# Performance work log

Measured on AMD Instinct MI355X. Metric: run time of the kernel, lower is better.

The kernel has to match this reference:

```python
import jax, jax.numpy as jnp
import numpy as np

MEAN = 0.1307
SIGMA = 0.3081
BINARY_ITER = 10
SIG_SCALE = 5.0


def spu(x):
    # SPU(x) = x^2 - 0.5 for x >= 0, sigmoid(-x) - 1 for x < 0 (continuous at 0)
    return jnp.where(x >= 0, x * x - 0.5, jax.nn.sigmoid(-x) - 1.0)


def joining_line(x1, y1, x2, y2):
    slope = (y2 - y1) / (x2 - x1)
    return slope, y2 - slope * x2


def parabola_tangent(x):
    return 2.0 * x, -x * x - 0.5


def parabola_tangent_through(x1, y1):
    D = 4.0 * x1 * x1 - 4.0 * y1 - 2.0
    x2 = (2.0 * x1 + jnp.sqrt(jnp.clip(D, 0.0))) / 2.0
    return parabola_tangent(x2)


def sigmoid_tangent(x):
    s = jax.nn.sigmoid(x)
    slope = -s * (1.0 - s)
    return slope, -s - slope * x


def binary_search_point(lx, ux, uy):
    L = lx
    R = jnp.zeros_like(lx)
    for _ in range(BINARY_ITER):  # fixed 10-iteration search, unrolled
        m = 0.5 * (L + R)
        sm, im = sigmoid_tangent(m)
        mask = sm * ux + im - uy > 0
        L = jnp.where(mask, m, L)
        R = jnp.where(mask, R, m)
    return L


def line_to_constraint(slope, intercept):
    # [n, n+1]: diagonal slope matrix with intercept as last column (matches torch diagflat/cat)
    return jnp.concatenate([jnp.diagflat(slope), intercept[:, None]], axis=1)


def analyze_affine(W, b, ub, lb):
    constr = jnp.concatenate([W, b[:, None]], axis=1)
    bu = jnp.where(W > 0, ub[None, :], lb[None, :])
    bl = jnp.where(W > 0, lb[None, :], ub[None, :])
    return constr, jnp.einsum('ij,ij->i', bu, W) + b, jnp.einsum('ij,ij->i', bl, W) + b


def analyze_spu(ux, lx):
    uy = spu(ux)
    ly = spu(lx)
    new_ub = jnp.maximum(uy, ly)
    sj, ij = joining_line(lx, ly, ux, uy)
    right = lx > 0
    left = ux <= 0
    crossing = (~left) & (~right)
    # learned positions at their (fresh) init: sigmoid(0) -> midpoint
    mid = 0.5 * (ux + lx)
    sp, ip = parabola_tangent(mid)
    ssm, ism = sigmoid_tangent(mid)
    new_lb = jnp.where(crossing, jnp.full_like(uy, -0.5), jnp.minimum(uy, ly))
    # crossing-case lower constraint
    spu_, ipu = parabola_tangent(ux)
    limit = spu_ * lx + ipu
    clm = (jnp.abs(lx) > ux).astype(lx.dtype)
    clp = jax.nn.sigmoid((clm - 0.5) * 2.0 * SIG_SCALE) * (ly - limit) + limit
    ptm = clp < -0.5
    spt, ipt = parabola_tangent_through(lx, clp)
    sjn, ijn = joining_line(lx, clp, jnp.zeros_like(lx), jnp.full_like(lx, -0.5))
    s_cl = jnp.where(ptm, spt, sjn)
    i_cl = jnp.where(ptm, ipt, ijn)
    # crossing-case upper constraint
    ssl, isl = sigmoid_tangent(lx)
    stv = ssl * ux + isl - uy
    L = binary_search_point(lx, ux, uy)
    scp = jax.nn.sigmoid(-SIG_SCALE) * (L - lx) + lx
    ssc, isc = sigmoid_tangent(scp)
    up_mask = stv > 0
    s_cu = jnp.where(up_mask, ssc, sj)
    i_cu = jnp.where(up_mask, isc, ij)
    rf = right.astype(lx.dtype)
    lf = left.astype(lx.dtype)
    cf = crossing.astype(lx.dtype)
    us = rf * sj + lf * ssm + cf * s_cu
    ui = rf * ij + lf * ism + cf * i_cu
    ls = rf * sp + lf * sj + cf * s_cl
    li = rf * ip + lf * ij + cf * i_cl
    return line_to_constraint(us, ui), line_to_constraint(ls, li), new_ub, new_lb


def back_substitute(uc, lc, ub, lb):
    cu, cl = uc[-1], lc[-1]
    for pu, pl in zip(uc[-2::-1], lc[-2::-1]):
        # where(curr>0, prev_upper, prev_lower) contracted with curr == split pos/neg matmuls
        Wu, bu = cu[:, :-1], cu[:, -1]
        cu = jnp.maximum(Wu, 0.0) @ pu + jnp.minimum(Wu, 0.0) @ pl
        cu = cu.at[:, -1].add(bu)
        Wl, bl = cl[:, :-1], cl[:, -1]
        cl = jnp.maximum(Wl, 0.0) @ pl + jnp.minimum(Wl, 0.0) @ pu
        cl = cl.at[:, -1].add(bl)
    return jnp.minimum(ub, cu[:, 0]), jnp.maximum(lb, cl[:, 0])


def setup_inputs() -> dict:
    key = jax.random.key(0)
    ks = jax.random.split(key, 9)
    d_in, h, d_out = 784, 2048, 10
    inputs = jax.random.uniform(ks[0], (d_in,), dtype=jnp.float32)
    eps = jnp.float32(0.05)
    w1 = jax.random.normal(ks[1], (h, d_in), dtype=jnp.float32) / np.sqrt(d_in).astype(np.float32)
    b1 = jax.random.normal(ks[2], (h,), dtype=jnp.float32) * 0.1
    w2 = jax.random.normal(ks[3], (h, h), dtype=jnp.float32) / np.sqrt(h).astype(np.float32)
    b2 = jax.random.normal(ks[4], (h,), dtype=jnp.float32) * 0.1
    w3 = jax.random.normal(ks[5], (h, h), dtype=jnp.float32) / np.sqrt(h).astype(np.float32)
    b3 = jax.random.normal(ks[6], (h,), dtype=jnp.float32) * 0.1
    w4 = jax.random.normal(ks[7], (d_out, h), dtype=jnp.float32) / np.sqrt(h).astype(np.float32)
    b4 = jax.random.normal(ks[8], (d_out,), dtype=jnp.float32) * 0.1
    return {"inputs": inputs, "eps": eps, "w1": w1, "b1": b1, "w2": w2, "b2": b2,
            "w3": w3, "b3": b3, "w4": w4, "b4": b4}


def reference(inputs, eps, w1, b1, w2, b2, w3, b3, w4, b4):
    ub = [jnp.clip(inputs + eps, None, 1.0)]
    lb = [jnp.clip(inputs - eps, 0.0)]
    # normalization layer: applied in place to bounds and input constraint ([784,1])
    uc = [((ub[0] - MEAN) / SIGMA)[:, None]]
    lc = [((lb[0] - MEAN) / SIGMA)[:, None]]
    ub[0] = (ub[0] - MEAN) / SIGMA
    lb[0] = (lb[0] - MEAN) / SIGMA
    weights = [(w1, b1), (w2, b2), (w3, b3), (w4, b4)]
    for i, (W, b) in enumerate(weights):
        c, u, l = analyze_affine(W, b, ub[-1], lb[-1])
        uc.append(c)
        lc.append(c)
        ub.append(u)
        lb.append(l)
        u, l = back_substitute(uc, lc, ub[-1], lb[-1])
        ub[-1], lb[-1] = u, l
        if i < len(weights) - 1:
            cu_, cl_, u, l = analyze_spu(ub[-1], lb[-1])
            uc.append(cu_)
            lc.append(cl_)
            ub.append(u)
            lb.append(l)
            u, l = back_substitute(uc, lc, ub[-1], lb[-1])
            ub[-1], lb[-1] = u, l
    return lb[-1].min()
```

## Files before the change

kernel.cpp:

```cpp
#include <hip/hip_runtime.h>
#include <cstdint>
#include <cstddef>

#define MEAN_C 0.1307f
#define SIGMA_C 0.3081f
#define SIG_SCALE_C 5.0f

typedef __bf16 bf16_t;
typedef __bf16 bf16x8 __attribute__((ext_vector_type(8)));
typedef __bf16 bf16x4 __attribute__((ext_vector_type(4)));
typedef float f32x4 __attribute__((ext_vector_type(4)));

__device__ __forceinline__ f32x4 mfma16(bf16x8 a, bf16x8 b, f32x4 c) {
    return __builtin_amdgcn_mfma_f32_16x16x32_bf16(a, b, c, 0, 0, 0);
}

typedef const __attribute__((address_space(1))) void* gvp;
typedef __attribute__((address_space(3))) void* lvp;
__device__ __forceinline__ void g2l16(const void* g, void* l) {
    __builtin_amdgcn_global_load_lds((gvp)g, (lvp)l, 16, 0, 0);
}

__device__ __forceinline__ size_t swz(int r, int k, int ktiles) {
    return (((size_t)(r >> 4) * ktiles + (k >> 5)) << 9)
         + (((k >> 3) & 3) << 7) + ((r & 15) << 3) + (k & 7);
}

#define KTILES 64


__device__ __forceinline__ float sigmoidf_(float x) {
    if (x >= 0.f) { float e = __expf(-x); return 1.f / (1.f + e); }
    float e = __expf(x); return e / (1.f + e);
}

__device__ __forceinline__ float spu_f(float x) {
    return (x >= 0.f) ? (x * x - 0.5f) : (sigmoidf_(-x) - 1.f);
}

__device__ __forceinline__ float wave_sum(float a) {
    #pragma unroll
    for (int o = 32; o > 0; o >>= 1) a += __shfl_xor(a, o, 64);
    return a;
}


__global__ __launch_bounds__(256) void k_interval_affine(
        const float* __restrict__ W, const float* __restrict__ b,
        const float* __restrict__ U, const float* __restrict__ L,
        int m, int nrows, float* __restrict__ uo, float* __restrict__ lo) {
    int r = (blockIdx.x << 2) + (threadIdx.x >> 6);
    if (r >= nrows) return;
    int lane = threadIdx.x & 63;
    const f32x4* Wr = (const f32x4*)(W + (size_t)r * m);
    const f32x4* U4 = (const f32x4*)U;
    const f32x4* L4 = (const f32x4*)L;
    int nf4 = m >> 2;
    float au = 0.f, al = 0.f;
    for (int j = lane; j < nf4; j += 64) {
        f32x4 wv = Wr[j], uu = U4[j], ll = L4[j];
        #pragma unroll
        for (int u = 0; u < 4; ++u) {
            float w = wv[u];
            float hi = (w > 0.f) ? uu[u] : ll[u];
            float lo2 = (w > 0.f) ? ll[u] : uu[u];
            au = fmaf(w, hi, au);
            al = fmaf(w, lo2, al);
        }
    }
    au = wave_sum(au); al = wave_sum(al);
    if (lane == 0) { uo[r] = au + b[r]; lo[r] = al + b[r]; }
}

__global__ void k_spu2(const float* __restrict__ iU, const float* __restrict__ iL,
                       const float* __restrict__ vraw, int n,
                       float* __restrict__ us, float* __restrict__ ui,
                       float* __restrict__ ls, float* __restrict__ li,
                       float* __restrict__ pU, float* __restrict__ pL) {
    int i = blockIdx.x * blockDim.x + threadIdx.x;
    if (i >= n) return;
    float ux = fminf(iU[i], vraw[i]);
    float lx = fmaxf(iL[i], vraw[n + i]);
    float uy = spu_f(ux), ly = spu_f(lx);
    float new_ub = fmaxf(uy, ly);
    float sj = (uy - ly) / (ux - lx);
    float ij = uy - sj * ux;
    bool right = lx > 0.f;
    bool left = ux <= 0.f;
    bool crossing = (!left) && (!right);
    float mid = 0.5f * (ux + lx);
    float sp = 2.f * mid, ip = -mid * mid - 0.5f;
    float sm = sigmoidf_(mid);
    float ssm = -sm * (1.f - sm);
    float ism = -sm - ssm * mid;
    float new_lb = crossing ? -0.5f : fminf(uy, ly);
    float spu_s = 2.f * ux, ipu = -ux * ux - 0.5f;
    float limit = spu_s * lx + ipu;
    float clm = (fabsf(lx) > ux) ? 1.f : 0.f;
    float clp = sigmoidf_((clm - 0.5f) * 2.f * SIG_SCALE_C) * (ly - limit) + limit;
    bool ptm = clp < -0.5f;
    float D = 4.f * lx * lx - 4.f * clp - 2.f;
    float x2 = (2.f * lx + sqrtf(fmaxf(D, 0.f))) * 0.5f;
    float spt = 2.f * x2, ipt = -x2 * x2 - 0.5f;
    float sjn = (clp + 0.5f) / lx;
    float ijn = -0.5f;
    float s_cl = ptm ? spt : sjn;
    float i_cl = ptm ? ipt : ijn;
    float sl = sigmoidf_(lx);
    float ssl = -sl * (1.f - sl);
    float isl = -sl - ssl * lx;
    float stv = ssl * ux + isl - uy;
    float Lb = lx, Rb = 0.f;
    #pragma unroll
    for (int t = 0; t < 10; ++t) {
        float mm = 0.5f * (Lb + Rb);
        float smm = sigmoidf_(mm);
        float sms = -smm * (1.f - smm);
        float smi = -smm - sms * mm;
        bool mask = (sms * ux + smi - uy) > 0.f;
        Lb = mask ? mm : Lb;
        Rb = mask ? Rb : mm;
    }
    float scp = sigmoidf_(-SIG_SCALE_C) * (Lb - lx) + lx;
    float sc = sigmoidf_(scp);
    float ssc = -sc * (1.f - sc);
    float isc = -sc - ssc * scp;
    bool up = stv > 0.f;
    float s_cu = up ? ssc : sj;
    float i_cu = up ? isc : ij;
    float usv, uiv, lsv, liv;
    if (right)      { usv = sj;   uiv = ij;   lsv = sp;   liv = ip;   }
    else if (left)  { usv = ssm;  uiv = ism;  lsv = sj;   liv = ij;   }
    else            { usv = s_cu; uiv = i_cu; lsv = s_cl; liv = i_cl; }
    us[i] = usv; ui[i] = uiv; ls[i] = lsv; li[i] = liv;
    float vu = vraw[(usv >= 0.f) ? i : n + i];
    float vl = vraw[(lsv >= 0.f) ? n + i : i];
    pU[i] = fminf(new_ub, usv * vu + uiv);
    pL[i] = fmaxf(new_lb, lsv * vl + liv);
}


__global__ __launch_bounds__(256) void k_wT3(
        const float* __restrict__ W1, const float* __restrict__ W2,
        const float* __restrict__ W3,
        bf16_t* __restrict__ W1t, bf16_t* __restrict__ W2t, bf16_t* __restrict__ W3t,
        const float* __restrict__ x, const float* __restrict__ eps,
        float* __restrict__ ubn, float* __restrict__ lbn) {
    __shared__ bf16_t t[64][72];
    int z = blockIdx.z;
    const float* W; int N, ldw; bf16_t* Wt;
    if (z == 0)      { W = W2; N = 2048; ldw = 2048; Wt = W2t; }
    else if (z == 1) { W = W3; N = 2048; ldw = 2048; Wt = W3t; }
    else {
        W = W1; N = 784; ldw = 784; Wt = W1t;
        if (blockIdx.y >= 14) {
            if (blockIdx.y == 14 && blockIdx.x == 0) {
                for (int i = threadIdx.x; i < 896; i += 256) {
                    if (i >= 784) { ubn[i] = 0.f; lbn[i] = 0.f; }
                    else {
                        float e = eps[0];
                        float ub = fminf(x[i] + e, 1.f);
                        float lb = fmaxf(x[i] - e, 0.f);
                        ubn[i] = (ub - MEAN_C) / SIGMA_C;
                        lbn[i] = (lb - MEAN_C) / SIGMA_C;
                    }
                }
            }
            return;
        }
    }
    int k0 = blockIdx.x * 64, n0 = blockIdx.y * 64;
    int tid = threadIdx.x;
    int r = tid >> 2;
    int c0 = (tid & 3) * 16;
    const float* Wr = W + (size_t)(k0 + r) * ldw;
    #pragma unroll
    for (int c = 0; c < 16; ++c) {
        int gn = n0 + c0 + c;
        float vv = (gn < N) ? Wr[gn] : 0.f;
        t[c0 + c][r] = (bf16_t)vv;
    }
    __syncthreads();
    #pragma unroll
    for (int p = 0; p < 2; ++p) {
        int c = tid + p * 256;
        int lr = c & 63, lq = c >> 6;
        bf16x8 v;
        #pragma unroll
        for (int u = 0; u < 8; ++u) v[u] = t[lr][lq * 8 + u];
        *(bf16x8*)(Wt + swz(n0 + lr, k0 + lq * 8, KTILES)) = v;
    }
}

__global__ __launch_bounds__(256) void k_prep16(
        const float* __restrict__ W, const float* __restrict__ b, int n,
        const float* __restrict__ cus, const float* __restrict__ cui,
        const float* __restrict__ cls, const float* __restrict__ cli,
        const float* __restrict__ bvec,
        const float* __restrict__ U, const float* __restrict__ L,
        bf16_t* __restrict__ Ab, float* __restrict__ av,
        float* __restrict__ iU, float* __restrict__ iL) {
    int rt = blockIdx.x;
    int tid = threadIdx.x, lane = tid & 63, wid = tid >> 6;
    int mrow = lane & 15, q = lane >> 4;
    int r = rt * 16 + mrow;
    bool act = r < 2 * n;
    bool isU = r < n;
    int i = act ? (isU ? r : r - n) : 0;
    float gate = act ? 1.f : 0.f;
    const float* Wr = W + (size_t)i * 2048;
    const float* ps = isU ? cus : cls;
    const float* ns = isU ? cls : cus;
    const float* yi = isU ? cui : cli;
    const float* zi = isU ? cli : cui;
    const float* hi = isU ? U : L;
    const float* lo = isU ? L : U;
    float a = 0.f, a2 = 0.f;
    bf16_t* Abase = Ab + ((size_t)rt * KTILES) * 512 + lane * 8;
    for (int kt = wid; kt < KTILES; kt += 4) {
        int k0 = kt * 32 + q * 8;
        bf16x8 ov;
        #pragma unroll
        for (int h = 0; h < 2; ++h) {
            int kb = k0 + 4 * h;
            f32x4 wv = *(const f32x4*)(Wr + kb);
            f32x4 p0 = *(const f32x4*)(ps + kb);
            f32x4 q0 = *(const f32x4*)(ns + kb);
            f32x4 y0 = *(const f32x4*)(yi + kb);
            f32x4 z0 = *(const f32x4*)(zi + kb);
            f32x4 c0 = *(const f32x4*)(bvec + kb);
            f32x4 h0 = *(const f32x4*)(hi + kb);
            f32x4 l0 = *(const f32x4*)(lo + kb);
            #pragma unroll
            for (int u = 0; u < 4; ++u) {
                float w = gate * wv[u];
                float pos = fmaxf(w, 0.f), neg = fminf(w, 0.f);
                float mx = pos * p0[u] + neg * q0[u];
                ov[4 * h + u] = (bf16_t)mx;
                a += pos * y0[u] + neg * z0[u] + mx * c0[u];
                a2 += pos * h0[u] + neg * l0[u];
            }
        }
        *(bf16x8*)(Abase + (size_t)kt * 512) = ov;
    }
    a += __shfl_xor(a, 16, 64);  a += __shfl_xor(a, 32, 64);
    a2 += __shfl_xor(a2, 16, 64); a2 += __shfl_xor(a2, 32, 64);
    __shared__ float sh[2][4][16];
    if (lane < 16) { sh[0][wid][lane] = a; sh[1][wid][lane] = a2; }
    __syncthreads();
    if (tid < 16) {
        int r2 = rt * 16 + tid;
        float ta = sh[0][0][tid] + sh[0][1][tid] + sh[0][2][tid] + sh[0][3][tid];
        float tb = sh[1][0][tid] + sh[1][1][tid] + sh[1][2][tid] + sh[1][3][tid];
        if (r2 < 2 * n) {
            bool isU2 = r2 < n;
            int i2 = isU2 ? r2 : r2 - n;
            av[r2] = ta + b[i2];
            if (isU2) iU[i2] = tb + b[i2];
            else      iL[i2] = tb + b[i2];
        } else {
            av[r2] = 0.f;
        }
    }
}

__global__ __launch_bounds__(256) void k_colmix16(
        const bf16_t* __restrict__ Cb, int ldc, int splits, size_t sstride, int n,
        int tpb,
        const float* __restrict__ cus, const float* __restrict__ cui,
        const float* __restrict__ cls, const float* __restrict__ cli,
        const float* __restrict__ bvec,
        bf16_t* __restrict__ Ab, float* __restrict__ av) {
    int rt = blockIdx.x;
    int kt0 = blockIdx.y * tpb;
    int tid = threadIdx.x, lane = tid & 63, wid = tid >> 6;
    int mrow = lane & 15, q = lane >> 4;
    int r = rt * 16 + mrow;
    bool isU = r < n;
    const bf16_t* Cr = Cb + (size_t)r * ldc;
    const float* ps = isU ? cus : cls;
    const float* ns = isU ? cls : cus;
    const float* yi = isU ? cui : cli;
    const float* zi = isU ? cli : cui;
    float a = 0.f;
    bf16_t* Abase = Ab + ((size_t)rt * KTILES) * 512 + lane * 8;
    for (int kt = kt0 + wid; kt < kt0 + tpb; kt += 4) {
        int k0 = kt * 32 + q * 8;
        float wsum[8] = {0.f, 0.f, 0.f, 0.f, 0.f, 0.f, 0.f, 0.f};
        for (int s = 0; s < splits; ++s) {
            bf16x8 v = *(const bf16x8*)(Cr + s * sstride + k0);
            #pragma unroll
            for (int u = 0; u < 8; ++u) wsum[u] += (float)v[u];
        }
        f32x4 p0 = *(const f32x4*)(ps + k0), p1 = *(const f32x4*)(ps + k0 + 4);
        f32x4 q0 = *(const f32x4*)(ns + k0), q1 = *(const f32x4*)(ns + k0 + 4);
        f32x4 y0 = *(const f32x4*)(yi + k0), y1 = *(const f32x4*)(yi + k0 + 4);
        f32x4 z0 = *(const f32x4*)(zi + k0), z1 = *(const f32x4*)(zi + k0 + 4);
        f32x4 c0 = *(const f32x4*)(bvec + k0), c1 = *(const f32x4*)(bvec + k0 + 4);
        bf16x8 ov;
        #pragma unroll
        for (int u = 0; u < 4; ++u) {
            float w = wsum[u];
            float pos = fmaxf(w, 0.f), neg = fminf(w, 0.f);
            float mx = pos * p0[u] + neg * q0[u];
            ov[u] = (bf16_t)mx;
            a += pos * y0[u] + neg * z0[u] + mx * c0[u];
        }
        #pragma unroll
        for (int u = 0; u < 4; ++u) {
            float w = wsum[4 + u];
            float pos = fmaxf(w, 0.f), neg = fminf(w, 0.f);
            float mx = pos * p1[u] + neg * q1[u];
            ov[4 + u] = (bf16_t)mx;
            a += pos * y1[u] + neg * z1[u] + mx * c1[u];
        }
        *(bf16x8*)(Abase + (size_t)kt * 512) = ov;
    }
    a += __shfl_xor(a, 16, 64);
    a += __shfl_xor(a, 32, 64);
    __shared__ float sh[4][16];
    if (lane < 16) sh[wid][lane] = a;
    __syncthreads();
    if (tid < 16) {
        float tot = sh[0][tid] + sh[1][tid] + sh[2][tid] + sh[3][tid];
        atomicAdd(&av[rt * 16 + tid], tot);
    }
}

__global__ __launch_bounds__(640) void k_reduce16f(
        const bf16_t* __restrict__ Cb, int ldc, int m, int n,
        int splits, size_t sstride,
        const float* __restrict__ av,
        const float* __restrict__ ubn, const float* __restrict__ lbn,
        const float* __restrict__ iL,
        float* __restrict__ out) {
    __shared__ float sbl[16];
    int tid = threadIdx.x, lane = tid & 63, wv = tid >> 6;
    int nch = m >> 3;
    int i = wv;
    int r = n + i;
    const bf16_t* Cr = Cb + (size_t)r * ldc;
    const float* p = lbn;
    const float* q = ubn;
    float a = 0.f;
    for (int c = lane; c < nch; c += 64) {
        float wsum[8] = {0.f, 0.f, 0.f, 0.f, 0.f, 0.f, 0.f, 0.f};
        for (int s = 0; s < splits; ++s) {
            bf16x8 v = *(const bf16x8*)(Cr + s * sstride + c * 8);
            #pragma unroll
            for (int u = 0; u < 8; ++u) wsum[u] += (float)v[u];
        }
        f32x4 p0 = *(const f32x4*)(p + c * 8), p1 = *(const f32x4*)(p + c * 8 + 4);
        f32x4 q0 = *(const f32x4*)(q + c * 8), q1 = *(const f32x4*)(q + c * 8 + 4);
        #pragma unroll
        for (int u = 0; u < 4; ++u) {
            a += fmaxf(wsum[u], 0.f) * p0[u] + fminf(wsum[u], 0.f) * q0[u];
            a += fmaxf(wsum[4 + u], 0.f) * p1[u] + fminf(wsum[4 + u], 0.f) * q1[u];
        }
    }
    a = wave_sum(a);
    if (lane == 0) sbl[i] = fmaxf(iL[i], a + av[r]);
    __syncthreads();
    if (tid < 64) {
        float v = 3.4e38f;
        for (int j = lane; j < n; j += 64) v = fminf(v, sbl[j]);
        #pragma unroll
        for (int o = 32; o > 0; o >>= 1) v = fminf(v, __shfl_down(v, o, 64));
        if (lane == 0) out[0] = v;
    }
}


#define GEMM_PIPE()                                                            \
    int tid = threadIdx.x, lane = tid & 63, w = tid >> 6;                      \
    int wm = w & 1, wn = w >> 1;                                               \
    const int nsteps = nk * 2;                                                 \
    f32x4 acc[4][4];                                                           \
    _Pragma("unroll")                                                          \
    for (int i = 0; i < 4; ++i)                                                \
        _Pragma("unroll")                                                      \
        for (int j = 0; j < 4; ++j) acc[i][j] = (f32x4){0.f, 0.f, 0.f, 0.f};   \
    auto stage = [&](int js) {                                                 \
        int b = js & 3;                                                        \
        size_t go = (size_t)js * 512;                                          \
        bf16_t* la = &As4[b * 4096 + w * 512];                                 \
        bf16_t* lb = &Bs4[b * 4096 + w * 512];                                 \
        g2l16(a0 + go, la);   g2l16(a1 + go, la + 2048);                       \
        g2l16(b0 + go, lb);   g2l16(b1 + go, lb + 2048);                       \
    };                                                                         \
    stage(0); stage(1); stage(2);                                              \
    asm volatile("s_waitcnt vmcnt(8)" ::: "memory");                           \
    __builtin_amdgcn_s_barrier();                                              \
    for (int j = 0; j < nsteps; ++j) {                                         \
        int b = j & 3;                                                         \
        const bf16_t* cA = &As4[b * 4096];                                     \
        const bf16_t* cB = &Bs4[b * 4096];                                     \
        bf16x8 af[4], bq[4];                                                   \
        _Pragma("unroll")                                                      \
        for (int i = 0; i < 4; ++i) {                                          \
            af[i] = *(const bf16x8*)(cA + (wm * 4 + i) * 512 + lane * 8);      \
            bq[i] = *(const bf16x8*)(cB + (wn * 4 + i) * 512 + lane * 8);      \
        }                                                                      \
        if (j + 3 < nsteps) stage(j + 3);                                      \
        _Pragma("unroll")                                                      \
        for (int i = 0; i < 4; ++i)                                            \
            _Pragma("unroll")                                                  \
            for (int jj = 0; jj < 4; ++jj)                                     \
                acc[i][jj] = mfma16(bq[jj], af[i], acc[i][jj]);                \
        int rem = nsteps - 2 - j;                                              \
        if (rem >= 2)      asm volatile("s_waitcnt vmcnt(8)" ::: "memory");    \
        else if (rem == 1) asm volatile("s_waitcnt vmcnt(4)" ::: "memory");    \
        else               asm volatile("s_waitcnt vmcnt(0)" ::: "memory");    \
        __builtin_amdgcn_s_barrier();                                          \
    }

__global__ __launch_bounds__(256) void k_gemm16(
        const bf16_t* __restrict__ A, const bf16_t* __restrict__ Bt,
        bf16_t* __restrict__ C, int ldc, size_t sstride, int nk) {
    __shared__ __align__(16) bf16_t As4[16384];
    __shared__ __align__(16) bf16_t Bs4[16384];
    int tr0 = blockIdx.y * 8, tc0 = blockIdx.x * 8;
    int kt0 = blockIdx.z * nk * 2;
    int wtmp = threadIdx.x >> 6, ltmp = threadIdx.x & 63;
    const bf16_t* a0 = A + (((size_t)(tr0 + wtmp)     * KTILES + kt0) << 9) + ltmp * 8;
    const bf16_t* a1 = A + (((size_t)(tr0 + wtmp + 4) * KTILES + kt0) << 9) + ltmp * 8;
    const bf16_t* b0 = Bt + (((size_t)(tc0 + wtmp)     * KTILES + kt0) << 9) + ltmp * 8;
    const bf16_t* b1 = Bt + (((size_t)(tc0 + wtmp + 4) * KTILES + kt0) << 9) + ltmp * 8;
    GEMM_PIPE()
    bf16_t* Cz = C + (size_t)blockIdx.z * sstride;
    int orow = lane & 15, ocol = (lane >> 4) * 4;
    size_t row0 = (size_t)blockIdx.y * 128;
    size_t col0 = (size_t)blockIdx.x * 128;
    #pragma unroll
    for (int i = 0; i < 4; ++i) {
        size_t gr = row0 + wm * 64 + i * 16 + orow;
        #pragma unroll
        for (int j = 0; j < 4; ++j) {
            size_t gc = col0 + wn * 64 + j * 16 + ocol;
            bf16x4 v;
            #pragma unroll
            for (int rg = 0; rg < 4; ++rg) v[rg] = (bf16_t)acc[i][j][rg];
            *(bf16x4*)(Cz + gr * (size_t)ldc + gc) = v;
        }
    }
}

__global__ __launch_bounds__(256) void k_gemm16_mix(
        const bf16_t* __restrict__ A, const bf16_t* __restrict__ Bt, int n,
        const float* __restrict__ cus, const float* __restrict__ cui,
        const float* __restrict__ cls, const float* __restrict__ cli,
        const float* __restrict__ bvec,
        bf16_t* __restrict__ Ab2, float* __restrict__ av, int nk) {
    __shared__ __align__(16) bf16_t As4[16384];
    __shared__ __align__(16) bf16_t Bs4[16384];
    __shared__ float asum[2][128];
    int wg = (int)(blockIdx.y * gridDim.x + blockIdx.x);
    int xcd = wg & 7, idx = wg >> 3;
    int bm = (xcd & 3) * 8 + (idx & 7);
    int bn = (xcd >> 2) * 8 + (idx >> 3);
    int tr0 = bm * 8, tc0 = bn * 8;
    int wtmp = threadIdx.x >> 6, ltmp = threadIdx.x & 63;
    const bf16_t* a0 = A + (((size_t)(tr0 + wtmp)     * KTILES) << 9) + ltmp * 8;
    const bf16_t* a1 = A + (((size_t)(tr0 + wtmp + 4) * KTILES) << 9) + ltmp * 8;
    const bf16_t* b0 = Bt + (((size_t)(tc0 + wtmp)     * KTILES) << 9) + ltmp * 8;
    const bf16_t* b1 = Bt + (((size_t)(tc0 + wtmp + 4) * KTILES) << 9) + ltmp * 8;
    GEMM_PIPE()
    size_t row0 = (size_t)bm * 128;
    size_t col0 = (size_t)bn * 128;
    bool isU = (int)row0 < n;
    const float* ps = isU ? cus : cls;
    const float* ns = isU ? cls : cus;
    const float* yi = isU ? cui : cli;
    const float* zi = isU ? cli : cui;
    int orow = lane & 15, ocol = (lane >> 4) * 4;
    #pragma unroll
    for (int i = 0; i < 4; ++i) {
        int gr = (int)row0 + wm * 64 + i * 16 + orow;
        float ra = 0.f;
        #pragma unroll
        for (int j = 0; j < 4; ++j) {
            int gc = (int)col0 + wn * 64 + j * 16 + ocol;
            f32x4 p0 = *(const f32x4*)(ps + gc);
            f32x4 q0 = *(const f32x4*)(ns + gc);
            f32x4 y0 = *(const f32x4*)(yi + gc);
            f32x4 z0 = *(const f32x4*)(zi + gc);
            f32x4 c0 = *(const f32x4*)(bvec + gc);
            bf16x4 ov;
            #pragma unroll
            for (int rg = 0; rg < 4; ++rg) {
                float v = acc[i][j][rg];
                float pos = fmaxf(v, 0.f), neg = fminf(v, 0.f);
                float mx = pos * p0[rg] + neg * q0[rg];
                ov[rg] = (bf16_t)mx;
                ra += pos * y0[rg] + neg * z0[rg] + mx * c0[rg];
            }
            *(bf16x4*)(Ab2 + swz(gr, gc, KTILES)) = ov;
        }
        ra += __shfl_xor(ra, 16, 64);
        ra += __shfl_xor(ra, 32, 64);
        if (lane < 16) asum[wn][wm * 64 + i * 16 + lane] = ra;
    }
    __syncthreads();
    if (tid < 128) atomicAdd(&av[row0 + tid], asum[0][tid] + asum[1][tid]);
}

__global__ __launch_bounds__(256) void k_gemm16_red(
        const bf16_t* __restrict__ A, const bf16_t* __restrict__ Bt, int n,
        const float* __restrict__ ubn, const float* __restrict__ lbn,
        float* __restrict__ av, int nk) {
    __shared__ __align__(16) bf16_t As4[16384];
    __shared__ __align__(16) bf16_t Bs4[16384];
    __shared__ float asum[2][128];
    int tr0 = blockIdx.x * 8, tc0 = blockIdx.y * 8;
    int wtmp = threadIdx.x >> 6, ltmp = threadIdx.x & 63;
    const bf16_t* a0 = A + (((size_t)(tr0 + wtmp)     * KTILES) << 9) + ltmp * 8;
    const bf16_t* a1 = A + (((size_t)(tr0 + wtmp + 4) * KTILES) << 9) + ltmp * 8;
    const bf16_t* b0 = Bt + (((size_t)(tc0 + wtmp)     * KTILES) << 9) + ltmp * 8;
    const bf16_t* b1 = Bt + (((size_t)(tc0 + wtmp + 4) * KTILES) << 9) + ltmp * 8;
    GEMM_PIPE()
    size_t row0 = (size_t)blockIdx.x * 128;
    size_t col0 = (size_t)blockIdx.y * 128;
    bool isU = (int)row0 < n;
    const float* p = isU ? ubn : lbn;
    const float* q = isU ? lbn : ubn;
    int ocol = (lane >> 4) * 4;
    #pragma unroll
    for (int i = 0; i < 4; ++i) {
        float ra = 0.f;
        #pragma unroll
        for (int j = 0; j < 4; ++j) {
            int gc = (int)col0 + wn * 64 + j * 16 + ocol;
            f32x4 p0 = *(const f32x4*)(p + gc);
            f32x4 q0 = *(const f32x4*)(q + gc);
            #pragma unroll
            for (int rg = 0; rg < 4; ++rg) {
                float v = acc[i][j][rg];
                ra += fmaxf(v, 0.f) * p0[rg] + fminf(v, 0.f) * q0[rg];
            }
        }
        ra += __shfl_xor(ra, 16, 64);
        ra += __shfl_xor(ra, 32, 64);
        if (lane < 16) asum[wn][wm * 64 + i * 16 + lane] = ra;
    }
    __syncthreads();
    if (tid < 128) atomicAdd(&av[row0 + tid], asum[0][tid] + asum[1][tid]);
}


extern "C" void kernel_launch(void* const* d_in, const int* in_sizes, int n_in,
                              void* d_out, int out_size, void* d_ws, size_t ws_size,
                              hipStream_t stream) {
    (void)in_sizes; (void)n_in; (void)out_size; (void)ws_size;
    const float* x   = (const float*)d_in[0];
    const float* eps = (const float*)d_in[1];
    const float* W1  = (const float*)d_in[2];
    const float* B1  = (const float*)d_in[3];
    const float* W2  = (const float*)d_in[4];
    const float* B2  = (const float*)d_in[5];
    const float* W3  = (const float*)d_in[6];
    const float* B3  = (const float*)d_in[7];
    const float* W4  = (const float*)d_in[8];
    const float* B4  = (const float*)d_in[9];
    float* out = (float*)d_out;

    const int H = 2048, DIN = 784, DOUT = 10;
    const int NP1 = 896;
    const int MP4 = 128;

    float* ws = (float*)d_ws;
    size_t off = 0;
    auto alloc = [&](size_t nf) -> float* {
        float* p = ws + off;
        off += (nf + 3) & ~(size_t)3;
        return p;
    };
    float* ubn = alloc(NP1);
    float* lbn = alloc(NP1);
    float* vraw1 = alloc(2 * H);
    float* us1 = alloc(H); float* ui1 = alloc(H); float* ls1 = alloc(H); float* li1 = alloc(H);
    float* pU1 = alloc(H); float* pL1 = alloc(H);
    float* iU2 = alloc(H); float* iL2 = alloc(H);
    float* us2 = alloc(H); float* ui2 = alloc(H); float* ls2 = alloc(H); float* li2 = alloc(H);
    float* pU2 = alloc(H); float* pL2 = alloc(H);
    float* iU3 = alloc(H); float* iL3 = alloc(H);
    float* us3 = alloc(H); float* ui3 = alloc(H); float* ls3 = alloc(H); float* li3 = alloc(H);
    float* pU3 = alloc(H); float* pL3 = alloc(H);
    float* iU4 = alloc(32); float* iL4 = alloc(32);
    float* av  = alloc(2 * H);
    bf16_t* Ab  = (bf16_t*)alloc((size_t)2 * H * H / 2);
    bf16_t* Ab2 = (bf16_t*)alloc((size_t)2 * H * H / 2);
    bf16_t* W1t = (bf16_t*)alloc((size_t)NP1 * H / 2);
    bf16_t* W2t = (bf16_t*)alloc((size_t)H * H / 2);
    bf16_t* W3t = (bf16_t*)alloc((size_t)H * H / 2);
    bf16_t* Cs  = (bf16_t*)alloc((size_t)16 * MP4 * H / 2);

    dim3 blk(256);

    k_wT3<<<dim3(32, 32, 3), blk, 0, stream>>>(W1, W2, W3, W1t, W2t, W3t,
                                               x, eps, ubn, lbn);

    size_t ss4H = (size_t)MP4 * H;
    size_t ss4N = (size_t)MP4 * NP1;

    k_interval_affine<<<dim3(H / 4), blk, 0, stream>>>(W1, B1, ubn, lbn, DIN, H,
                                                       vraw1, vraw1 + H);
    k_spu2<<<dim3(H / 256), blk, 0, stream>>>(vraw1, vraw1 + H, vraw1, H,
        us1, ui1, ls1, li1, pU1, pL1);

    k_prep16<<<dim3(2 * H / 16), blk, 0, stream>>>(W2, B2, H,
        us1, ui1, ls1, li1, B1, pU1, pL1, Ab, av, iU2, iL2);
    k_gemm16_red<<<dim3(2 * H / 128, NP1 / 128), blk, 0, stream>>>(Ab, W1t, H,
        ubn, lbn, av, KTILES / 2);
    k_spu2<<<dim3(H / 256), blk, 0, stream>>>(iU2, iL2, av, H,
        us2, ui2, ls2, li2, pU2, pL2);

    k_prep16<<<dim3(2 * H / 16), blk, 0, stream>>>(W3, B3, H,
        us2, ui2, ls2, li2, B2, pU2, pL2, Ab, av, iU3, iL3);
    k_gemm16_mix<<<dim3(2 * H / 128, H / 128), blk, 0, stream>>>(Ab, W2t, H,
        us1, ui1, ls1, li1, B1, Ab2, av, KTILES / 2);
    k_gemm16_red<<<dim3(2 * H / 128, NP1 / 128), blk, 0, stream>>>(Ab2, W1t, H,
        ubn, lbn, av, KTILES / 2);
    k_spu2<<<dim3(H / 256), blk, 0, stream>>>(iU3, iL3, av, H,
        us3, ui3, ls3, li3, pU3, pL3);

    k_prep16<<<dim3(MP4 / 16), blk, 0, stream>>>(W4, B4, DOUT,
        us3, ui3, ls3, li3, B3, pU3, pL3, Ab, av, iU4, iL4);
    k_gemm16<<<dim3(H / 128, MP4 / 128, 16), blk, 0, stream>>>(Ab, W3t, Cs, H, ss4H, 2);
    k_colmix16<<<dim3(MP4 / 16, 8), blk, 0, stream>>>(Cs, H, 16, ss4H, DOUT, KTILES / 8,
        us2, ui2, ls2, li2, B2, Ab2, av);
    k_gemm16<<<dim3(H / 128, MP4 / 128, 16), blk, 0, stream>>>(Ab2, W2t, Cs, H, ss4H, 2);
    k_colmix16<<<dim3(MP4 / 16, 8), blk, 0, stream>>>(Cs, H, 16, ss4H, DOUT, KTILES / 8,
        us1, ui1, ls1, li1, B1, Ab, av);
    k_gemm16<<<dim3(NP1 / 128, MP4 / 128, 16), blk, 0, stream>>>(Ab, W1t, Cs, NP1, ss4N, 2);
    k_reduce16f<<<dim3(1), dim3(640), 0, stream>>>(Cs, NP1, DIN, DOUT, 16, ss4N,
        av, ubn, lbn, iL4, out);
}
```

Baseline: 356.0 us.

## Restructure GEMM pipeline to double-buffered 64-wide K steps, remap red tiles, shrink SPU blocks

```diff
diff --git a/kernel.cpp b/kernel.cpp
--- a/kernel.cpp
+++ b/kernel.cpp
@@ -374,51 +374,58 @@
 #define GEMM_PIPE()                                                            \
     int tid = threadIdx.x, lane = tid & 63, w = tid >> 6;                      \
     int wm = w & 1, wn = w >> 1;                                               \
-    const int nsteps = nk * 2;                                                 \
     f32x4 acc[4][4];                                                           \
     _Pragma("unroll")                                                          \
     for (int i = 0; i < 4; ++i)                                                \
         _Pragma("unroll")                                                      \
         for (int j = 0; j < 4; ++j) acc[i][j] = (f32x4){0.f, 0.f, 0.f, 0.f};   \
-    auto stage = [&](int js) {                                                 \
-        int b = js & 3;                                                        \
-        size_t go = (size_t)js * 512;                                          \
-        bf16_t* la = &As4[b * 4096 + w * 512];                                 \
-        bf16_t* lb = &Bs4[b * 4096 + w * 512];                                 \
-        g2l16(a0 + go, la);   g2l16(a1 + go, la + 2048);                       \
-        g2l16(b0 + go, lb);   g2l16(b1 + go, lb + 2048);                       \
+    auto stage = [&](int kk) {                                                 \
+        int b = kk & 1;                                                        \
+        size_t go = (size_t)kk * 1024;                                         \
+        bf16_t* la = &As2[b * 8192 + w * 1024];                                \
+        bf16_t* lb = &Bs2[b * 8192 + w * 1024];                                \
+        g2l16(a0 + go, la);          g2l16(a0 + go + 512, la + 512);           \
+        g2l16(a1 + go, la + 4096);   g2l16(a1 + go + 512, la + 4608);          \
+        g2l16(b0 + go, lb);          g2l16(b0 + go + 512, lb + 512);           \
+        g2l16(b1 + go, lb + 4096);   g2l16(b1 + go + 512, lb + 4608);          \
     };                                                                         \
-    stage(0); stage(1); stage(2);                                              \
+    stage(0); stage(1);                                                        \
     asm volatile("s_waitcnt vmcnt(8)" ::: "memory");                           \
     __builtin_amdgcn_s_barrier();                                              \
-    for (int j = 0; j < nsteps; ++j) {                                         \
-        int b = j & 3;                                                         \
-        const bf16_t* cA = &As4[b * 4096];                                     \
-        const bf16_t* cB = &Bs4[b * 4096];                                     \
-        bf16x8 af[4], bq[4];                                                   \
+    for (int kk = 0; kk < nk; ++kk) {                                          \
+        const bf16_t* cA = &As2[(kk & 1) * 8192];                              \
+        const bf16_t* cB = &Bs2[(kk & 1) * 8192];                              \
+        bf16x8 af0[4], af1[4], bq0[4], bq1[4];                                 \
         _Pragma("unroll")                                                      \
         for (int i = 0; i < 4; ++i) {                                          \
-            af[i] = *(const bf16x8*)(cA + (wm * 4 + i) * 512 + lane * 8);      \
-            bq[i] = *(const bf16x8*)(cB + (wn * 4 + i) * 512 + lane * 8);      \
+            af0[i] = *(const bf16x8*)(cA + (wm * 4 + i) * 1024 + lane * 8);    \
+            af1[i] = *(const bf16x8*)(cA + (wm * 4 + i) * 1024 + 512 + lane * 8); \
+            bq0[i] = *(const bf16x8*)(cB + (wn * 4 + i) * 1024 + lane * 8);    \
+            bq1[i] = *(const bf16x8*)(cB + (wn * 4 + i) * 1024 + 512 + lane * 8); \
         }                                                                      \
-        if (j + 3 < nsteps) stage(j + 3);                                      \
+        asm volatile("s_waitcnt lgkmcnt(0)" ::: "memory");                     \
+        __builtin_amdgcn_s_barrier();                                          \
+        if (kk + 2 < nk) stage(kk + 2);                                        \
         _Pragma("unroll")                                                      \
         for (int i = 0; i < 4; ++i)                                            \
             _Pragma("unroll")                                                  \
-            for (int jj = 0; jj < 4; ++jj)                                     \
-                acc[i][jj] = mfma16(bq[jj], af[i], acc[i][jj]);                \
-        int rem = nsteps - 2 - j;                                              \
-        if (rem >= 2)      asm volatile("s_waitcnt vmcnt(8)" ::: "memory");    \
-        else if (rem == 1) asm volatile("s_waitcnt vmcnt(4)" ::: "memory");    \
-        else               asm volatile("s_waitcnt vmcnt(0)" ::: "memory");    \
+            for (int j = 0; j < 4; ++j)                                        \
+                acc[i][j] = mfma16(bq0[j], af0[i], acc[i][j]);                 \
+        _Pragma("unroll")                                                      \
+        for (int i = 0; i < 4; ++i)                                            \
+            _Pragma("unroll")                                                  \
+            for (int j = 0; j < 4; ++j)                                        \
+                acc[i][j] = mfma16(bq1[j], af1[i], acc[i][j]);                 \
+        if (kk + 2 < nk) asm volatile("s_waitcnt vmcnt(8)" ::: "memory");      \
+        else             asm volatile("s_waitcnt vmcnt(0)" ::: "memory");      \
         __builtin_amdgcn_s_barrier();                                          \
     }
 
 __global__ __launch_bounds__(256) void k_gemm16(
         const bf16_t* __restrict__ A, const bf16_t* __restrict__ Bt,
         bf16_t* __restrict__ C, int ldc, size_t sstride, int nk) {
-    __shared__ __align__(16) bf16_t As4[16384];
-    __shared__ __align__(16) bf16_t Bs4[16384];
+    __shared__ __align__(16) bf16_t As2[16384];
+    __shared__ __align__(16) bf16_t Bs2[16384];
     int tr0 = blockIdx.y * 8, tc0 = blockIdx.x * 8;
     int kt0 = blockIdx.z * nk * 2;
     int wtmp = threadIdx.x >> 6, ltmp = threadIdx.x & 63;
@@ -451,8 +458,8 @@
         const float* __restrict__ cls, const float* __restrict__ cli,
         const float* __restrict__ bvec,
         bf16_t* __restrict__ Ab2, float* __restrict__ av, int nk) {
-    __shared__ __align__(16) bf16_t As4[16384];
-    __shared__ __align__(16) bf16_t Bs4[16384];
+    __shared__ __align__(16) bf16_t As2[16384];
+    __shared__ __align__(16) bf16_t Bs2[16384];
     __shared__ float asum[2][128];
     int wg = (int)(blockIdx.y * gridDim.x + blockIdx.x);
     int xcd = wg & 7, idx = wg >> 3;
@@ -508,18 +515,21 @@
         const bf16_t* __restrict__ A, const bf16_t* __restrict__ Bt, int n,
         const float* __restrict__ ubn, const float* __restrict__ lbn,
         float* __restrict__ av, int nk) {
-    __shared__ __align__(16) bf16_t As4[16384];
-    __shared__ __align__(16) bf16_t Bs4[16384];
+    __shared__ __align__(16) bf16_t As2[16384];
+    __shared__ __align__(16) bf16_t Bs2[16384];
     __shared__ float asum[2][128];
-    int tr0 = blockIdx.x * 8, tc0 = blockIdx.y * 8;
+    int wg = (int)(blockIdx.y * gridDim.x + blockIdx.x);
+    int id = (wg & 7) * 28 + (wg >> 3);
+    int bm = id / 7, bn = id % 7;
+    int tr0 = bm * 8, tc0 = bn * 8;
     int wtmp = threadIdx.x >> 6, ltmp = threadIdx.x & 63;
     const bf16_t* a0 = A + (((size_t)(tr0 + wtmp)     * KTILES) << 9) + ltmp * 8;
     const bf16_t* a1 = A + (((size_t)(tr0 + wtmp + 4) * KTILES) << 9) + ltmp * 8;
     const bf16_t* b0 = Bt + (((size_t)(tc0 + wtmp)     * KTILES) << 9) + ltmp * 8;
     const bf16_t* b1 = Bt + (((size_t)(tc0 + wtmp + 4) * KTILES) << 9) + ltmp * 8;
     GEMM_PIPE()
-    size_t row0 = (size_t)blockIdx.x * 128;
-    size_t col0 = (size_t)blockIdx.y * 128;
+    size_t row0 = (size_t)bm * 128;
+    size_t col0 = (size_t)bn * 128;
     bool isU = (int)row0 < n;
     const float* p = isU ? ubn : lbn;
     const float* q = isU ? lbn : ubn;
@@ -604,14 +614,14 @@
 
     k_interval_affine<<<dim3(H / 4), blk, 0, stream>>>(W1, B1, ubn, lbn, DIN, H,
                                                        vraw1, vraw1 + H);
-    k_spu2<<<dim3(H / 256), blk, 0, stream>>>(vraw1, vraw1 + H, vraw1, H,
+    k_spu2<<<dim3(H / 64), dim3(64), 0, stream>>>(vraw1, vraw1 + H, vraw1, H,
         us1, ui1, ls1, li1, pU1, pL1);
 
     k_prep16<<<dim3(2 * H / 16), blk, 0, stream>>>(W2, B2, H,
         us1, ui1, ls1, li1, B1, pU1, pL1, Ab, av, iU2, iL2);
     k_gemm16_red<<<dim3(2 * H / 128, NP1 / 128), blk, 0, stream>>>(Ab, W1t, H,
         ubn, lbn, av, KTILES / 2);
-    k_spu2<<<dim3(H / 256), blk, 0, stream>>>(iU2, iL2, av, H,
+    k_spu2<<<dim3(H / 64), dim3(64), 0, stream>>>(iU2, iL2, av, H,
         us2, ui2, ls2, li2, pU2, pL2);
 
     k_prep16<<<dim3(2 * H / 16), blk, 0, stream>>>(W3, B3, H,
@@ -620,7 +630,7 @@
         us1, ui1, ls1, li1, B1, Ab2, av, KTILES / 2);
     k_gemm16_red<<<dim3(2 * H / 128, NP1 / 128), blk, 0, stream>>>(Ab2, W1t, H,
         ubn, lbn, av, KTILES / 2);
-    k_spu2<<<dim3(H / 256), blk, 0, stream>>>(iU3, iL3, av, H,
+    k_spu2<<<dim3(H / 64), dim3(64), 0, stream>>>(iU3, iL3, av, H,
         us3, ui3, ls3, li3, pU3, pL3);
 
     k_prep16<<<dim3(MP4 / 16), blk, 0, stream>>>(W4, B4, DOUT,
```

Result: no change. 350.7 us (-1.5%).
